# Kernel optimization log

Hardware: AMD Instinct MI355X
Metric: run time of the kernel (lower is better)

The kernel has to match this reference:

```python
import jax, jax.numpy as jnp
import numpy as np

D_MODEL = 1024
NUM_HEADS = 16
HEAD_DIM = D_MODEL // NUM_HEADS


def setup_inputs() -> dict:
    key = jax.random.key(0)
    ks = jax.random.split(key, 5)
    scale = 1.0 / np.sqrt(D_MODEL)
    x = jax.random.normal(ks[0], (2, 2048, D_MODEL), dtype=jnp.float32)
    Wqkv = jax.random.normal(ks[1], (D_MODEL, 3 * D_MODEL), dtype=jnp.float32) * scale
    bqkv = jax.random.normal(ks[2], (3 * D_MODEL,), dtype=jnp.float32) * 0.02
    Wout = jax.random.normal(ks[3], (D_MODEL, D_MODEL), dtype=jnp.float32) * scale
    bout = jax.random.normal(ks[4], (D_MODEL,), dtype=jnp.float32) * 0.02
    return {"x": x, "Wqkv": Wqkv, "bqkv": bqkv, "Wout": Wout, "bout": bout}


def reference(x, Wqkv, bqkv, Wout, bout):
    B, T, D = x.shape
    H, Hd = NUM_HEADS, HEAD_DIM
    # fused QKV projection: [B,T,3D] -> [3,B,H,T,Hd]
    qkv = (x @ Wqkv + bqkv).reshape(B, T, 3, H, Hd).transpose(2, 0, 3, 1, 4)
    q, k, v = qkv[0], qkv[1], qkv[2]
    # scaled dot-product attention with full TxT scores (faithful to source)
    scores = jnp.einsum("bhqd,bhkd->bhqk", q, k) / np.sqrt(Hd).astype(np.float32)
    weights = jax.nn.softmax(scores, axis=-1)
    context = jnp.einsum("bhqk,bhkd->bhqd", weights, v)
    context = context.transpose(0, 2, 1, 3).reshape(B, T, D)
    return context @ Wout + bout
```

## Files before the change

kernel.cpp:

```cpp
#include <hip/hip_runtime.h>
#include <hip/hip_bf16.h>

#define D_MODEL 1024
#define T_SEQ   2048
#define BATCH   2
#define NHEADS  16
#define HDIM    64
#define QKVSZ   (BATCH * NHEADS * T_SEQ * HDIM)

#define SCALE_Q 0.18033688011112042f

typedef __bf16 bf16_t;
typedef bf16_t bf16x8  __attribute__((ext_vector_type(8)));
typedef float  f32x4   __attribute__((ext_vector_type(4)));
typedef float  f32x16  __attribute__((ext_vector_type(16)));
typedef unsigned uint32x4 __attribute__((ext_vector_type(4)));

#if __has_builtin(__builtin_amdgcn_exp2f)
#define EXP2F(x) __builtin_amdgcn_exp2f(x)
#else
#define EXP2F(x) exp2f(x)
#endif

__device__ __forceinline__ unsigned short f2bf(float f) {
    union { float f; unsigned u; } v; v.f = f;
    unsigned u = v.u;
    u += 0x7FFFu + ((u >> 16) & 1u);
    return (unsigned short)(u >> 16);
}

__device__ __forceinline__ unsigned pkbf(float a, float b) {
    unsigned r;
    asm("v_cvt_pk_bf16_f32 %0, %1, %2" : "=v"(r) : "v"(a), "v"(b));
    return r;
}

__device__ __forceinline__ void gload16(const unsigned short* g, unsigned short* l) {
    __builtin_amdgcn_global_load_lds(
        (const __attribute__((address_space(1))) void*)g,
        (__attribute__((address_space(3))) void*)l,
        16, 0, 0);
}

__global__ void cvt_f32_bf16(const float* __restrict__ src,
                             unsigned short* __restrict__ dst, int n4) {
    int i = blockIdx.x * blockDim.x + threadIdx.x;
    if (i < n4) {
        float4 v = reinterpret_cast<const float4*>(src)[i];
        ushort4 o;
        o.x = f2bf(v.x); o.y = f2bf(v.y); o.z = f2bf(v.z); o.w = f2bf(v.w);
        reinterpret_cast<ushort4*>(dst)[i] = o;
    }
}

__global__ __launch_bounds__(256) void cvt_transpose(
    const float* __restrict__ src, unsigned short* __restrict__ dst, int K, int N)
{
    __shared__ unsigned short Ls[64][72];
    const int n0 = blockIdx.x * 64, k0 = blockIdx.y * 64;
    const int tid = threadIdx.x;
    #pragma unroll
    for (int it = 0; it < 4; ++it) {
        const int r = it * 16 + (tid >> 4);
        const int c = (tid & 15) * 4;
        float4 v = *reinterpret_cast<const float4*>(src + (size_t)(k0 + r) * N + n0 + c);
        Ls[c + 0][r] = f2bf(v.x); Ls[c + 1][r] = f2bf(v.y);
        Ls[c + 2][r] = f2bf(v.z); Ls[c + 3][r] = f2bf(v.w);
    }
    __syncthreads();
    #pragma unroll
    for (int it = 0; it < 2; ++it) {
        const int rn = it * 32 + (tid >> 3);
        const int ck = (tid & 7) * 8;
        *reinterpret_cast<uint4*>(dst + (size_t)(n0 + rn) * K + k0 + ck) =
            *reinterpret_cast<const uint4*>(&Ls[rn][ck]);
    }
}

__global__ __launch_bounds__(256) void transpose_v(
    const unsigned short* __restrict__ v, unsigned short* __restrict__ vt)
{
    __shared__ unsigned short Ls[64][72];
    const int t0 = blockIdx.x * 64;
    const size_t base = ((size_t)(blockIdx.z * NHEADS + blockIdx.y)) * T_SEQ * HDIM;
    const int tid = threadIdx.x;
    const int r  = tid >> 2;
    const int c0 = (tid & 3) * 16;
    unsigned short tmp[16];
    *reinterpret_cast<uint4*>(&tmp[0]) =
        *reinterpret_cast<const uint4*>(v + base + (size_t)(t0 + r) * HDIM + c0);
    *reinterpret_cast<uint4*>(&tmp[8]) =
        *reinterpret_cast<const uint4*>(v + base + (size_t)(t0 + r) * HDIM + c0 + 8);
    #pragma unroll
    for (int i = 0; i < 16; ++i) Ls[c0 + i][r] = tmp[i];
    __syncthreads();
    const int rn = tid >> 2;
    const int ck = (tid & 3) * 16;
    const int a  = ck >> 4;
    const int kb = 32 * (a >> 1) + 16 * (a & 1);
    unsigned short buf[16];
    #pragma unroll
    for (int i = 0; i < 16; ++i) {
        const int key = kb + 4 * (i >> 3) + 8 * ((i & 7) >> 2) + (i & 3);
        buf[i] = Ls[rn][key];
    }
    *reinterpret_cast<uint4*>(vt + base + (size_t)rn * T_SEQ + t0 + ck) =
        *reinterpret_cast<const uint4*>(&buf[0]);
    *reinterpret_cast<uint4*>(vt + base + (size_t)rn * T_SEQ + t0 + ck + 8) =
        *reinterpret_cast<const uint4*>(&buf[8]);
}

template<int MODE>
__global__ __launch_bounds__(256) void gemm128(
    const unsigned short* __restrict__ A,
    const unsigned short* __restrict__ BT,
    const float* __restrict__ bias,
    unsigned short* __restrict__ qkv,
    float* __restrict__ outf,
    int M, int N, int K)
{
    __shared__ unsigned short As[2][128 * 32];
    __shared__ unsigned short Bs[2][128 * 32];
    const int tid = threadIdx.x, wv = tid >> 6, lane = tid & 63;
    const int wr = wv >> 1, wc = wv & 1;

    const int P    = blockIdx.x;
    const int nwg  = gridDim.x;
    const int per  = nwg >> 3;
    const int L    = (P & 7) * per + (P >> 3);
    const int mt   = M >> 7;
    const int m0   = (L % mt) * 128;
    const int n0   = (L / mt) * 128;

    const int srow0 = 32 * wv + (lane >> 2);
    const int skc0  = (lane & 3) ^ ((srow0 >> 1) & 3);
    const int srow1 = srow0 + 16;
    const int skc1  = (lane & 3) ^ ((srow1 >> 1) & 3);

    #define GSTAGE(k0v, bf)                                                     \
        {                                                                       \
            gload16(A  + (size_t)(m0 + srow0) * K + (k0v) + skc0 * 8,           \
                    &As[bf][(32 * wv) * 32]);                                   \
            gload16(BT + (size_t)(n0 + srow0) * K + (k0v) + skc0 * 8,           \
                    &Bs[bf][(32 * wv) * 32]);                                   \
            gload16(A  + (size_t)(m0 + srow1) * K + (k0v) + skc1 * 8,           \
                    &As[bf][(32 * wv + 16) * 32]);                              \
            gload16(BT + (size_t)(n0 + srow1) * K + (k0v) + skc1 * 8,           \
                    &Bs[bf][(32 * wv + 16) * 32]);                              \
        }

    f32x4 acc[4][4] = {};

    GSTAGE(0, 0);
    __syncthreads();

    const int nk = K >> 5;
    for (int k = 0; k < nk; ++k) {
        const int cur = k & 1;
        if (k + 1 < nk) GSTAGE((k + 1) << 5, cur ^ 1);

        bf16x8 af[4], bfr[4];
        #pragma unroll
        for (int m = 0; m < 4; ++m) {
            const int row = 64 * wr + 16 * m + (lane & 15);
            const int s   = (lane >> 4) ^ ((row >> 1) & 3);
            af[m] = *reinterpret_cast<const bf16x8*>(&As[cur][row * 32 + s * 8]);
        }
        #pragma unroll
        for (int n = 0; n < 4; ++n) {
            const int row = 64 * wc + 16 * n + (lane & 15);
            const int s   = (lane >> 4) ^ ((row >> 1) & 3);
            bfr[n] = *reinterpret_cast<const bf16x8*>(&Bs[cur][row * 32 + s * 8]);
        }
        #pragma unroll
        for (int m = 0; m < 4; ++m)
            #pragma unroll
            for (int n = 0; n < 4; ++n)
                acc[m][n] = __builtin_amdgcn_mfma_f32_16x16x32_bf16(af[m], bfr[n], acc[m][n], 0, 0, 0);
        __syncthreads();
    }
    #undef GSTAGE

    const int rb = m0 + 64 * wr + ((lane >> 4) << 2);
    const int cb = n0 + 64 * wc + (lane & 15);
    #pragma unroll
    for (int n = 0; n < 4; ++n) {
        const int c = cb + 16 * n;
        const float bc = bias[c];
        #pragma unroll
        for (int m = 0; m < 4; ++m) {
            #pragma unroll
            for (int jr = 0; jr < 4; ++jr) {
                const int r = rb + 16 * m + jr;
                float val = acc[m][n][jr] + bc;
                if (MODE == 0) {
                    const int which = c >> 10;
                    const int rem = c & 1023;
                    const int h = rem >> 6, hd = rem & 63;
                    const int b = r >> 11, t = r & 2047;
                    if (which == 0) val *= SCALE_Q;
                    qkv[(size_t)which * QKVSZ + ((((size_t)b * NHEADS + h) * T_SEQ + t) << 6) + hd] = f2bf(val);
                } else {
                    outf[(size_t)r * N + c] = val;
                }
            }
        }
    }
}

__global__ __launch_bounds__(512) void attn32(
    const unsigned short* __restrict__ qb,
    const unsigned short* __restrict__ kb,
    const unsigned short* __restrict__ vtb,
    unsigned short* __restrict__ ctx)
{
    __shared__ unsigned short Ks[2][2][64 * 64];
    __shared__ unsigned short Vt[2][2][64 * 64];

    const int tid = threadIdx.x;
    const int wv = tid >> 6, lane = tid & 63;
    const int wg = wv >> 2, wl = wv & 3;
    const int ql = lane & 31;
    const int hi = lane >> 5;

    const int P    = blockIdx.x + 16 * blockIdx.y + 256 * blockIdx.z;
    const int xcd  = P & 7, slot = P >> 3;
    const int qt   = slot & 15;
    const int hidx = xcd * 4 + (slot >> 4);
    const int h    = hidx & 15, b = hidx >> 4;

    const size_t base = ((size_t)(b * NHEADS + h)) * T_SEQ * HDIM;
    const unsigned short* Kp  = kb  + base;
    const unsigned short* Vtp = vtb + base;
    const unsigned short* Qp  = qb  + base + ((size_t)qt * 128 + wl * 32 + ql) * HDIM;

    const bf16x8 qf0 = *reinterpret_cast<const bf16x8*>(Qp + 0  + hi * 8);
    const bf16x8 qf1 = *reinterpret_cast<const bf16x8*>(Qp + 16 + hi * 8);
    const bf16x8 qf2 = *reinterpret_cast<const bf16x8*>(Qp + 32 + hi * 8);
    const bf16x8 qf3 = *reinterpret_cast<const bf16x8*>(Qp + 48 + hi * 8);

    const int srow = lane >> 3;
    const int ssl  = lane & 7;
    #define STAGE(i, bf)                                                          \
        {                                                                         \
            _Pragma("unroll")                                                     \
            for (int ihalf = 0; ihalf < 2; ++ihalf) {                             \
                const int g2  = wl * 2 + ihalf;                                   \
                const int row = 8 * g2 + srow;                                    \
                const int sl  = ssl ^ (row & 7) ^ ((row >> 3) & 3);               \
                gload16(Kp  + (size_t)((wg * 16 + (i)) * 64 + row) * HDIM + sl * 8, \
                        &Ks[wg][bf][g2 * 512]);                                   \
                gload16(Vtp + (size_t)row * T_SEQ + (wg * 16 + (i)) * 64 + sl * 8, \
                        &Vt[wg][bf][g2 * 512]);                                   \
            }                                                                     \
        }

    STAGE(0, 0);
    __syncthreads();

    const int kx = (ql & 7) ^ ((ql >> 3) & 3);

    float m = -1e30f, l = 0.f;
    f32x16 o0 = {}, o1 = {};

    for (int i = 0; i < 16; ++i) {
        const int cur = i & 1;
        if (i + 1 < 16) STAGE(i + 1, cur ^ 1);

        f32x16 s0 = {}, s1 = {};
        __builtin_amdgcn_s_setprio(1);
        #pragma unroll
        for (int c = 0; c < 4; ++c) {
            const int sw = (2 * c + hi) ^ kx;
            const bf16x8 k0 = *reinterpret_cast<const bf16x8*>(&Ks[wg][cur][(ql)      * 64 + sw * 8]);
            const bf16x8 k1 = *reinterpret_cast<const bf16x8*>(&Ks[wg][cur][(32 + ql) * 64 + sw * 8]);
            const bf16x8 qc = (c == 0) ? qf0 : (c == 1) ? qf1 : (c == 2) ? qf2 : qf3;
            s0 = __builtin_amdgcn_mfma_f32_32x32x16_bf16(k0, qc, s0, 0, 0, 0);
            s1 = __builtin_amdgcn_mfma_f32_32x32x16_bf16(k1, qc, s1, 0, 0, 0);
        }
        __builtin_amdgcn_s_setprio(0);

        float a0 = fmaxf(s0[0], s0[4]), a1 = fmaxf(s0[1], s0[5]);
        float a2 = fmaxf(s0[2], s0[6]), a3 = fmaxf(s0[3], s0[7]);
        a0 = fmaxf(a0, fmaxf(s0[8],  s0[12]));  a1 = fmaxf(a1, fmaxf(s0[9],  s0[13]));
        a2 = fmaxf(a2, fmaxf(s0[10], s0[14])); a3 = fmaxf(a3, fmaxf(s0[11], s0[15]));
        a0 = fmaxf(a0, fmaxf(s1[0], s1[4]));   a1 = fmaxf(a1, fmaxf(s1[1], s1[5]));
        a2 = fmaxf(a2, fmaxf(s1[2], s1[6]));   a3 = fmaxf(a3, fmaxf(s1[3], s1[7]));
        a0 = fmaxf(a0, fmaxf(s1[8],  s1[12])); a1 = fmaxf(a1, fmaxf(s1[9],  s1[13]));
        a2 = fmaxf(a2, fmaxf(s1[10], s1[14])); a3 = fmaxf(a3, fmaxf(s1[11], s1[15]));
        float mx = fmaxf(fmaxf(a0, a1), fmaxf(a2, a3));
        mx = fmaxf(mx, __shfl_xor(mx, 32));

        if (__any(mx > m + 8.0f)) {
            const float mn = fmaxf(m, mx);
            const float sc = EXP2F(m - mn);
            l *= sc; m = mn;
            #pragma unroll
            for (int r = 0; r < 16; ++r) { o0[r] *= sc; o1[r] *= sc; }
        }

        #pragma unroll
        for (int r = 0; r < 16; ++r) s0[r] = EXP2F(s0[r] - m);
        #pragma unroll
        for (int r = 0; r < 16; ++r) s1[r] = EXP2F(s1[r] - m);
        float b0 = 0.f, b1 = 0.f, b2 = 0.f, b3 = 0.f;
        #pragma unroll
        for (int r = 0; r < 16; r += 4) {
            b0 += s0[r]; b1 += s0[r + 1]; b2 += s0[r + 2]; b3 += s0[r + 3];
            b0 += s1[r]; b1 += s1[r + 1]; b2 += s1[r + 2]; b3 += s1[r + 3];
        }
        float rs = (b0 + b1) + (b2 + b3);
        l += rs + __shfl_xor(rs, 32);

        __builtin_amdgcn_s_setprio(1);
        #pragma unroll
        for (int kc = 0; kc < 4; ++kc) {
            uint32x4 fw;
            if (kc == 0) {
                fw.x = pkbf(s0[0], s0[1]);   fw.y = pkbf(s0[2], s0[3]);
                fw.z = pkbf(s0[4], s0[5]);   fw.w = pkbf(s0[6], s0[7]);
            } else if (kc == 1) {
                fw.x = pkbf(s0[8], s0[9]);   fw.y = pkbf(s0[10], s0[11]);
                fw.z = pkbf(s0[12], s0[13]); fw.w = pkbf(s0[14], s0[15]);
            } else if (kc == 2) {
                fw.x = pkbf(s1[0], s1[1]);   fw.y = pkbf(s1[2], s1[3]);
                fw.z = pkbf(s1[4], s1[5]);   fw.w = pkbf(s1[6], s1[7]);
            } else {
                fw.x = pkbf(s1[8], s1[9]);   fw.y = pkbf(s1[10], s1[11]);
                fw.z = pkbf(s1[12], s1[13]); fw.w = pkbf(s1[14], s1[15]);
            }
            const bf16x8 pa = __builtin_bit_cast(bf16x8, fw);
            const int sw = (2 * kc + hi) ^ kx;
            const bf16x8 vva = *reinterpret_cast<const bf16x8*>(&Vt[wg][cur][(ql)      * 64 + sw * 8]);
            const bf16x8 vvb = *reinterpret_cast<const bf16x8*>(&Vt[wg][cur][(32 + ql) * 64 + sw * 8]);
            o0 = __builtin_amdgcn_mfma_f32_32x32x16_bf16(vva, pa, o0, 0, 0, 0);
            o1 = __builtin_amdgcn_mfma_f32_32x32x16_bf16(vvb, pa, o1, 0, 0, 0);
        }
        __builtin_amdgcn_s_setprio(0);

        __syncthreads();
    }
    #undef STAGE

    float* xo0  = (float*)&Ks[0][0][0];
    float* xo1m = (float*)&Vt[0][0][0];
    const int idx = wl * 64 + lane;
    if (wg == 1) {
        float* pa0 = xo0 + idx * 17;
        float* pb0 = xo1m + idx * 19;
        #pragma unroll
        for (int r = 0; r < 16; ++r) pa0[r] = o0[r];
        #pragma unroll
        for (int r = 0; r < 16; ++r) pb0[r] = o1[r];
        pb0[16] = m; pb0[17] = l;
    }
    __syncthreads();
    if (wg == 0) {
        const float* pa0 = xo0 + idx * 17;
        const float* pb0 = xo1m + idx * 19;
        const float m2 = pb0[16], l2 = pb0[17];
        const float mn = fmaxf(m, m2);
        const float ca = EXP2F(m - mn), cb = EXP2F(m2 - mn);
        const float invl = 1.0f / (l * ca + l2 * cb);
        const float fa = ca * invl, fb = cb * invl;

        const int t = qt * 128 + wl * 32 + ql;
        unsigned short* crow = ctx + ((size_t)b * T_SEQ + t) * D_MODEL + h * HDIM;
        #pragma unroll
        for (int r4 = 0; r4 < 4; ++r4) {
            const int d0 = 8 * r4 + 4 * hi;
            ushort4 w;
            w.x = f2bf(o0[4 * r4 + 0] * fa + pa0[4 * r4 + 0] * fb);
            w.y = f2bf(o0[4 * r4 + 1] * fa + pa0[4 * r4 + 1] * fb);
            w.z = f2bf(o0[4 * r4 + 2] * fa + pa0[4 * r4 + 2] * fb);
            w.w = f2bf(o0[4 * r4 + 3] * fa + pa0[4 * r4 + 3] * fb);
            *reinterpret_cast<ushort4*>(crow + d0) = w;
            w.x = f2bf(o1[4 * r4 + 0] * fa + pb0[4 * r4 + 0] * fb);
            w.y = f2bf(o1[4 * r4 + 1] * fa + pb0[4 * r4 + 1] * fb);
            w.z = f2bf(o1[4 * r4 + 2] * fa + pb0[4 * r4 + 2] * fb);
            w.w = f2bf(o1[4 * r4 + 3] * fa + pb0[4 * r4 + 3] * fb);
            *reinterpret_cast<ushort4*>(crow + 32 + d0) = w;
        }
    }
}

extern "C" void kernel_launch(void* const* d_in, const int* in_sizes, int n_in,
                              void* d_out, int out_size, void* d_ws, size_t ws_size,
                              hipStream_t stream) {
    const float* x    = (const float*)d_in[0];
    const float* Wqkv = (const float*)d_in[1];
    const float* bqkv = (const float*)d_in[2];
    const float* Wout = (const float*)d_in[3];
    const float* bout = (const float*)d_in[4];
    float* out = (float*)d_out;

    char* ws = (char*)d_ws;
    unsigned short* xb    = (unsigned short*)(ws);
    unsigned short* wqkvT = (unsigned short*)(ws + 8388608);
    unsigned short* woutT = (unsigned short*)(ws + 14680064);
    unsigned short* qkv   = (unsigned short*)(ws + 16777216);
    unsigned short* ctx   = (unsigned short*)(ws + 41943040);

    int n4 = (BATCH * T_SEQ * D_MODEL) / 4;
    cvt_f32_bf16<<<(n4 + 255) / 256, 256, 0, stream>>>(x, xb, n4);

    dim3 gt1(3 * D_MODEL / 64, D_MODEL / 64);
    cvt_transpose<<<gt1, 256, 0, stream>>>(Wqkv, wqkvT, D_MODEL, 3 * D_MODEL);
    dim3 gt2(D_MODEL / 64, D_MODEL / 64);
    cvt_transpose<<<gt2, 256, 0, stream>>>(Wout, woutT, D_MODEL, D_MODEL);

    gemm128<0><<<768, 256, 0, stream>>>(xb, wqkvT, bqkv, qkv, nullptr,
                                        BATCH * T_SEQ, 3 * D_MODEL, D_MODEL);

    dim3 gtv(T_SEQ / 64, NHEADS, BATCH);
    transpose_v<<<gtv, 256, 0, stream>>>(qkv + (size_t)2 * QKVSZ, xb);

    dim3 g2(T_SEQ / 128, NHEADS, BATCH);
    attn32<<<g2, 512, 0, stream>>>(qkv,
                                   qkv + (size_t)QKVSZ,
                                   xb,
                                   ctx);

    gemm128<1><<<256, 256, 0, stream>>>(ctx, woutT, bout, nullptr, out,
                                        BATCH * T_SEQ, D_MODEL, D_MODEL);
}
```

Measured before the change: 129.3 us.

## Deepen GEMM K-tile to 64 with prefetch-two pipeline and manual waitcnts

The projection GEMM now stages K tiles of 64 instead of 32 in a double-buffered LDS layout with an XOR swizzle over 8 chunks. It prefetches two tiles ahead and uses explicit vmcnt/lgkmcnt waits with raw s_barrier in place of __syncthreads. It also raises wave priority around the MFMA block. The goal is fewer barriers per unit of work and better overlap of global loads with MFMA. The cost is doubled LDS use, which may reduce occupancy, and fragile hand-counted waitcnt logic.

```diff
diff --git a/kernel.cpp b/kernel.cpp
--- a/kernel.cpp
+++ b/kernel.cpp
@@ -119,8 +119,8 @@
     float* __restrict__ outf,
     int M, int N, int K)
 {
-    __shared__ unsigned short As[2][128 * 32];
-    __shared__ unsigned short Bs[2][128 * 32];
+    __shared__ unsigned short As[2][128 * 64];
+    __shared__ unsigned short Bs[2][128 * 64];
     const int tid = threadIdx.x, wv = tid >> 6, lane = tid & 63;
     const int wr = wv >> 1, wc = wv & 1;
 
@@ -132,52 +132,69 @@
     const int m0   = (L % mt) * 128;
     const int n0   = (L / mt) * 128;
 
-    const int srow0 = 32 * wv + (lane >> 2);
-    const int skc0  = (lane & 3) ^ ((srow0 >> 1) & 3);
-    const int srow1 = srow0 + 16;
-    const int skc1  = (lane & 3) ^ ((srow1 >> 1) & 3);
-
-    #define GSTAGE(k0v, bf)                                                     \
+    const int srow = lane >> 3;
+    const int sch  = lane & 7;
+
+    #define GSTAGE(kt, bf)                                                      \
         {                                                                       \
-            gload16(A  + (size_t)(m0 + srow0) * K + (k0v) + skc0 * 8,           \
-                    &As[bf][(32 * wv) * 32]);                                   \
-            gload16(BT + (size_t)(n0 + srow0) * K + (k0v) + skc0 * 8,           \
-                    &Bs[bf][(32 * wv) * 32]);                                   \
-            gload16(A  + (size_t)(m0 + srow1) * K + (k0v) + skc1 * 8,           \
-                    &As[bf][(32 * wv + 16) * 32]);                              \
-            gload16(BT + (size_t)(n0 + srow1) * K + (k0v) + skc1 * 8,           \
-                    &Bs[bf][(32 * wv + 16) * 32]);                              \
-        }
+            _Pragma("unroll")                                                   \
+            for (int i = 0; i < 4; ++i) {                                       \
+                const int row = 32 * wv + 8 * i + srow;                         \
+                const int sc  = sch ^ (row & 7);                                \
+                gload16(A  + (size_t)(m0 + row) * K + (kt) * 64 + sc * 8,       \
+                        &As[bf][(32 * wv + 8 * i) * 64]);                       \
+                gload16(BT + (size_t)(n0 + row) * K + (kt) * 64 + sc * 8,       \
+                        &Bs[bf][(32 * wv + 8 * i) * 64]);                       \
+            }                                                                   \
+        }
+    #define VMCNT8  asm volatile("s_waitcnt vmcnt(8)" ::: "memory")
+    #define VMCNT0  asm volatile("s_waitcnt vmcnt(0)" ::: "memory")
+    #define LGKM0   asm volatile("s_waitcnt lgkmcnt(0)" ::: "memory")
 
     f32x4 acc[4][4] = {};
 
     GSTAGE(0, 0);
-    __syncthreads();
-
-    const int nk = K >> 5;
-    for (int k = 0; k < nk; ++k) {
-        const int cur = k & 1;
-        if (k + 1 < nk) GSTAGE((k + 1) << 5, cur ^ 1);
-
-        bf16x8 af[4], bfr[4];
-        #pragma unroll
-        for (int m = 0; m < 4; ++m) {
-            const int row = 64 * wr + 16 * m + (lane & 15);
-            const int s   = (lane >> 4) ^ ((row >> 1) & 3);
-            af[m] = *reinterpret_cast<const bf16x8*>(&As[cur][row * 32 + s * 8]);
-        }
-        #pragma unroll
-        for (int n = 0; n < 4; ++n) {
-            const int row = 64 * wc + 16 * n + (lane & 15);
-            const int s   = (lane >> 4) ^ ((row >> 1) & 3);
-            bfr[n] = *reinterpret_cast<const bf16x8*>(&Bs[cur][row * 32 + s * 8]);
-        }
-        #pragma unroll
-        for (int m = 0; m < 4; ++m)
+    GSTAGE(1, 1);
+    VMCNT8;
+    __builtin_amdgcn_s_barrier();
+
+    const int nk = K >> 6;
+    for (int kt = 0; kt < nk; ++kt) {
+        const int cur = kt & 1;
+
+        #pragma unroll
+        for (int kk = 0; kk < 2; ++kk) {
+            bf16x8 af[4], bfr[4];
             #pragma unroll
-            for (int n = 0; n < 4; ++n)
-                acc[m][n] = __builtin_amdgcn_mfma_f32_16x16x32_bf16(af[m], bfr[n], acc[m][n], 0, 0, 0);
-        __syncthreads();
+            for (int m = 0; m < 4; ++m) {
+                const int row = 64 * wr + 16 * m + (lane & 15);
+                const int c   = (4 * kk + (lane >> 4)) ^ (row & 7);
+                af[m] = *reinterpret_cast<const bf16x8*>(&As[cur][row * 64 + c * 8]);
+            }
+            #pragma unroll
+            for (int n = 0; n < 4; ++n) {
+                const int row = 64 * wc + 16 * n + (lane & 15);
+                const int c   = (4 * kk + (lane >> 4)) ^ (row & 7);
+                bfr[n] = *reinterpret_cast<const bf16x8*>(&Bs[cur][row * 64 + c * 8]);
+            }
+            __builtin_amdgcn_s_setprio(1);
+            #pragma unroll
+            for (int m = 0; m < 4; ++m)
+                #pragma unroll
+                for (int n = 0; n < 4; ++n)
+                    acc[m][n] = __builtin_amdgcn_mfma_f32_16x16x32_bf16(af[m], bfr[n], acc[m][n], 0, 0, 0);
+            __builtin_amdgcn_s_setprio(0);
+        }
+
+        LGKM0;
+        __builtin_amdgcn_s_barrier();
+        if (kt + 2 < nk) {
+            GSTAGE(kt + 2, cur);
+            VMCNT8;
+        } else {
+            VMCNT0;
+        }
+        __builtin_amdgcn_s_barrier();
     }
     #undef GSTAGE
 
```

Result: slower. 139.7 us (+8.1%).

## Merge prep conversions into one kernel and write transposed V from QKV GEMM epilogue

Applied to the files above, without the earlier changes.

Combines the x conversion and both weight convert-transposes into one prep launch indexed by block id. The QKV GEMM epilogue now writes V directly in the permuted transposed layout the attention kernel expects, which removes the separate transpose_v kernel and its extra read and write of V. This saves launch overhead and memory traffic. The cost is more scattered 8-byte stores in the GEMM epilogue for the V columns.

```diff
diff --git a/kernel.cpp b/kernel.cpp
--- a/kernel.cpp
+++ b/kernel.cpp
@@ -42,23 +42,37 @@
         16, 0, 0);
 }
 
-__global__ void cvt_f32_bf16(const float* __restrict__ src,
-                             unsigned short* __restrict__ dst, int n4) {
-    int i = blockIdx.x * blockDim.x + threadIdx.x;
-    if (i < n4) {
-        float4 v = reinterpret_cast<const float4*>(src)[i];
+__global__ __launch_bounds__(256) void prep(
+    const float* __restrict__ x,    unsigned short* __restrict__ xb,
+    const float* __restrict__ Wqkv, unsigned short* __restrict__ wqkvT,
+    const float* __restrict__ Wout, unsigned short* __restrict__ woutT)
+{
+    __shared__ unsigned short Ls[64][72];
+    const int blk = blockIdx.x;
+    const int tid = threadIdx.x;
+
+    if (blk < 4096) {
+        const int i = blk * 256 + tid;
+        float4 v = reinterpret_cast<const float4*>(x)[i];
         ushort4 o;
         o.x = f2bf(v.x); o.y = f2bf(v.y); o.z = f2bf(v.z); o.w = f2bf(v.w);
-        reinterpret_cast<ushort4*>(dst)[i] = o;
-    }
-}
-
-__global__ __launch_bounds__(256) void cvt_transpose(
-    const float* __restrict__ src, unsigned short* __restrict__ dst, int K, int N)
-{
-    __shared__ unsigned short Ls[64][72];
-    const int n0 = blockIdx.x * 64, k0 = blockIdx.y * 64;
-    const int tid = threadIdx.x;
+        reinterpret_cast<ushort4*>(xb)[i] = o;
+        return;
+    }
+
+    const float* src;
+    unsigned short* dst;
+    int n0, k0, N;
+    if (blk < 4864) {
+        const int idx = blk - 4096;
+        n0 = (idx % 48) * 64; k0 = (idx / 48) * 64;
+        src = Wqkv; dst = wqkvT; N = 3 * D_MODEL;
+    } else {
+        const int idx = blk - 4864;
+        n0 = (idx % 16) * 64; k0 = (idx / 16) * 64;
+        src = Wout; dst = woutT; N = D_MODEL;
+    }
+    const int K = D_MODEL;
     #pragma unroll
     for (int it = 0; it < 4; ++it) {
         const int r = it * 16 + (tid >> 4);
@@ -75,39 +89,6 @@
         *reinterpret_cast<uint4*>(dst + (size_t)(n0 + rn) * K + k0 + ck) =
             *reinterpret_cast<const uint4*>(&Ls[rn][ck]);
     }
-}
-
-__global__ __launch_bounds__(256) void transpose_v(
-    const unsigned short* __restrict__ v, unsigned short* __restrict__ vt)
-{
-    __shared__ unsigned short Ls[64][72];
-    const int t0 = blockIdx.x * 64;
-    const size_t base = ((size_t)(blockIdx.z * NHEADS + blockIdx.y)) * T_SEQ * HDIM;
-    const int tid = threadIdx.x;
-    const int r  = tid >> 2;
-    const int c0 = (tid & 3) * 16;
-    unsigned short tmp[16];
-    *reinterpret_cast<uint4*>(&tmp[0]) =
-        *reinterpret_cast<const uint4*>(v + base + (size_t)(t0 + r) * HDIM + c0);
-    *reinterpret_cast<uint4*>(&tmp[8]) =
-        *reinterpret_cast<const uint4*>(v + base + (size_t)(t0 + r) * HDIM + c0 + 8);
-    #pragma unroll
-    for (int i = 0; i < 16; ++i) Ls[c0 + i][r] = tmp[i];
-    __syncthreads();
-    const int rn = tid >> 2;
-    const int ck = (tid & 3) * 16;
-    const int a  = ck >> 4;
-    const int kb = 32 * (a >> 1) + 16 * (a & 1);
-    unsigned short buf[16];
-    #pragma unroll
-    for (int i = 0; i < 16; ++i) {
-        const int key = kb + 4 * (i >> 3) + 8 * ((i & 7) >> 2) + (i & 3);
-        buf[i] = Ls[rn][key];
-    }
-    *reinterpret_cast<uint4*>(vt + base + (size_t)rn * T_SEQ + t0 + ck) =
-        *reinterpret_cast<const uint4*>(&buf[0]);
-    *reinterpret_cast<uint4*>(vt + base + (size_t)rn * T_SEQ + t0 + ck + 8) =
-        *reinterpret_cast<const uint4*>(&buf[8]);
 }
 
 template<int MODE>
@@ -187,6 +168,30 @@
     for (int n = 0; n < 4; ++n) {
         const int c = cb + 16 * n;
         const float bc = bias[c];
+        if (MODE == 0 && (c >> 10) == 2) {
+            const int h  = (c & 1023) >> 6;
+            const int hd = c & 63;
+            #pragma unroll
+            for (int m = 0; m < 4; ++m) {
+                const int r4  = rb + 16 * m;
+                const int bb  = r4 >> 11;
+                const int tw  = r4 & 2047;
+                const int tile = tw >> 6;
+                const int key6 = tw & 63;
+                const int posb = 16 * ((((key6 >> 5) & 1) << 1) | ((key6 >> 4) & 1))
+                               + 8 * ((key6 >> 2) & 1) + 4 * ((key6 >> 3) & 1);
+                ushort4 w4;
+                w4.x = f2bf(acc[m][n][0] + bc);
+                w4.y = f2bf(acc[m][n][1] + bc);
+                w4.z = f2bf(acc[m][n][2] + bc);
+                w4.w = f2bf(acc[m][n][3] + bc);
+                unsigned short* vt = qkv + (size_t)2 * QKVSZ
+                    + ((((size_t)bb * NHEADS + h) * HDIM + hd) << 11)
+                    + tile * 64 + posb;
+                *reinterpret_cast<ushort4*>(vt) = w4;
+            }
+            continue;
+        }
         #pragma unroll
         for (int m = 0; m < 4; ++m) {
             #pragma unroll
@@ -401,24 +406,15 @@
     unsigned short* qkv   = (unsigned short*)(ws + 16777216);
     unsigned short* ctx   = (unsigned short*)(ws + 41943040);
 
-    int n4 = (BATCH * T_SEQ * D_MODEL) / 4;
-    cvt_f32_bf16<<<(n4 + 255) / 256, 256, 0, stream>>>(x, xb, n4);
-
-    dim3 gt1(3 * D_MODEL / 64, D_MODEL / 64);
-    cvt_transpose<<<gt1, 256, 0, stream>>>(Wqkv, wqkvT, D_MODEL, 3 * D_MODEL);
-    dim3 gt2(D_MODEL / 64, D_MODEL / 64);
-    cvt_transpose<<<gt2, 256, 0, stream>>>(Wout, woutT, D_MODEL, D_MODEL);
+    prep<<<5120, 256, 0, stream>>>(x, xb, Wqkv, wqkvT, Wout, woutT);
 
     gemm128<0><<<768, 256, 0, stream>>>(xb, wqkvT, bqkv, qkv, nullptr,
                                         BATCH * T_SEQ, 3 * D_MODEL, D_MODEL);
-
-    dim3 gtv(T_SEQ / 64, NHEADS, BATCH);
-    transpose_v<<<gtv, 256, 0, stream>>>(qkv + (size_t)2 * QKVSZ, xb);
 
     dim3 g2(T_SEQ / 128, NHEADS, BATCH);
     attn32<<<g2, 512, 0, stream>>>(qkv,
                                    qkv + (size_t)QKVSZ,
-                                   xb,
+                                   qkv + (size_t)2 * QKVSZ,
                                    ctx);
 
     gemm128<1><<<256, 256, 0, stream>>>(ctx, woutT, bout, nullptr, out,
```

New measurement: 120.8 us (median of 2 runs). 1.07x faster.
